# Kernel tuning notes

Measured on AMD Instinct MI355X. Metric: run time of the kernel, lower is better.

## Reference

```python
import jax, jax.numpy as jnp
import numpy as np

N = 50000      # nodes
E = 800000     # edges (avg degree 16)
F_IN = 128
H = 4          # heads
F_OUT = 64


def setup_inputs() -> dict:
    key = jax.random.key(0)
    ks = jax.random.split(key, 10)
    feat = jax.random.normal(ks[0], (N, F_IN), jnp.float32)
    src = jax.random.randint(ks[1], (E,), 0, N, dtype=jnp.int32)
    dst = jax.random.randint(ks[2], (E,), 0, N, dtype=jnp.int32)
    # fc: Linear(F_IN -> H*F_OUT, bias=False); torch weight layout [H*F_OUT, F_IN]
    fc_w = jax.random.normal(ks[3], (H * F_OUT, F_IN), jnp.float32) * (1.0 / np.sqrt(F_IN))
    # attention vectors live in input-feature space: (1, H, F_IN) -> store as (H, F_IN)
    attn_l = jax.random.normal(ks[4], (H, F_IN), jnp.float32) * 0.1
    attn_r = jax.random.normal(ks[5], (H, F_IN), jnp.float32) * 0.1
    attn_l1 = jax.random.normal(ks[6], (H, F_IN), jnp.float32) * 0.1
    attn_r1 = jax.random.normal(ks[7], (H, F_IN), jnp.float32) * 0.1
    bias = jax.random.normal(ks[8], (H * F_OUT,), jnp.float32) * 0.01
    return {"feat": feat, "src": src, "dst": dst, "fc_w": fc_w,
            "attn_l": attn_l, "attn_r": attn_r,
            "attn_l1": attn_l1, "attn_r1": attn_r1, "bias": bias}


def reference(feat, src, dst, fc_w, attn_l, attn_r, attn_l1, attn_r1, bias):
    n = feat.shape[0]
    h, f_out = attn_l.shape[0], fc_w.shape[0] // attn_l.shape[0]

    fs = feat[src]  # [E, F_in] gather
    fd = feat[dst]  # [E, F_in] gather

    # e1[e,h] = sum_f (feat[src]*attn_l)[h,f] * (feat[dst]*attn_r)[h,f]
    e1 = jnp.einsum('ef,ef,hf->eh', fs, fd, attn_l * attn_r)
    # e2 same with attn_l1/attn_r1
    e2 = jnp.einsum('ef,ef,hf->eh', fs, fd, attn_l1 * attn_r1)
    # e3 = ||feat[src]*attn_l1||^2 + ||feat[dst]*attn_r1||^2 (per node, then gathered)
    el2 = jnp.einsum('nf,hf->nh', feat * feat, attn_l1 * attn_l1)  # [N, H]
    er2 = jnp.einsum('nf,hf->nh', feat * feat, attn_r1 * attn_r1)  # [N, H]

    e = e1 - 2.0 * e2 + el2[src] + er2[dst]  # [E, H] squared-distance score

    # edge_softmax: softmax over incoming edges of each destination node
    m = jax.ops.segment_max(e, dst, num_segments=n)          # [N, H]
    ex = jnp.exp(e - m[dst])                                  # [E, H]
    denom = jax.ops.segment_sum(ex, dst, num_segments=n)     # [N, H]
    a = ex / denom[dst]                                       # [E, H]

    # feature projection then u_mul_e + sum aggregation
    ft = (feat @ fc_w.T).reshape(n, h, f_out)                 # [N, H, F_out]
    rst = jax.ops.segment_sum(ft[src] * a[:, :, None], dst, num_segments=n)

    return rst + bias.reshape(1, h, f_out)
```

## Files before the change

kernel.cpp:

```cpp
#include <hip/hip_runtime.h>

#define N_NODES 50000
#define F_IN    128
#define CAP     64
#define C_OUT   256
#define EDGE_BLOCKS 3125
#define W_BLOCKS    32
#define NODE_BLOCKS 12500

typedef short bf16x8 __attribute__((ext_vector_type(8)));
typedef float f32x4  __attribute__((ext_vector_type(4)));

__device__ __forceinline__ unsigned short f2bf(float f) {
    union { float f; unsigned u; } v; v.f = f;
    return (unsigned short)((v.u + 0x7FFFu + ((v.u >> 16) & 1u)) >> 16);
}
__device__ __forceinline__ float asf(unsigned u) { union { unsigned u; float f; } v; v.u = u; return v.f; }
__device__ __forceinline__ void unp8(uint4 u, float* f) {
    f[0] = asf(u.x << 16); f[1] = asf(u.x & 0xffff0000u);
    f[2] = asf(u.y << 16); f[3] = asf(u.y & 0xffff0000u);
    f[4] = asf(u.z << 16); f[5] = asf(u.z & 0xffff0000u);
    f[6] = asf(u.w << 16); f[7] = asf(u.w & 0xffff0000u);
}

__global__ __launch_bounds__(256) void k_prep(const float* __restrict__ feat,
                                              const float* __restrict__ fcw,
                                              const float* __restrict__ al1,
                                              const int* __restrict__ src,
                                              const int* __restrict__ dst,
                                              int* __restrict__ deg,
                                              int* __restrict__ esrc,
                                              unsigned short* __restrict__ fb16,
                                              unsigned short* __restrict__ wb16,
                                              float* __restrict__ el2) {
    int bid = blockIdx.x, t = threadIdx.x;
    if (bid < EDGE_BLOCKS) {
        int e = bid * 256 + t;
        int d = dst[e];
        int pos = atomicAdd(&deg[d], 1);
        if (pos < CAP) esrc[(size_t)d * CAP + pos] = src[e];
    } else if (bid < EDGE_BLOCKS + W_BLOCKS) {
        int j = (bid - EDGE_BLOCKS) * 256 + t;
        float4 v = ((const float4*)fcw)[j];
        ushort4 o = { f2bf(v.x), f2bf(v.y), f2bf(v.z), f2bf(v.w) };
        ((ushort4*)wb16)[j] = o;
    } else {
        int r = (bid - EDGE_BLOCKS - W_BLOCKS) * 4 + (t >> 6);
        int l = t & 63, h = l & 3, cb = l >> 2;
        const float4* fr = (const float4*)(feat + (size_t)r * F_IN + cb * 8);
        float4 f0 = fr[0], f1 = fr[1];
        const float4* ap = (const float4*)(al1 + h * F_IN + cb * 8);
        float4 a0 = ap[0], a1 = ap[1];
        float p = 0.f;
        p = fmaf(f0.x * f0.x, a0.x * a0.x, p);
        p = fmaf(f0.y * f0.y, a0.y * a0.y, p);
        p = fmaf(f0.z * f0.z, a0.z * a0.z, p);
        p = fmaf(f0.w * f0.w, a0.w * a0.w, p);
        p = fmaf(f1.x * f1.x, a1.x * a1.x, p);
        p = fmaf(f1.y * f1.y, a1.y * a1.y, p);
        p = fmaf(f1.z * f1.z, a1.z * a1.z, p);
        p = fmaf(f1.w * f1.w, a1.w * a1.w, p);
#pragma unroll
        for (int o = 4; o < 64; o <<= 1) p += __shfl_xor(p, o, 64);
        if (cb == 0) el2[r * 4 + h] = p;
        if (h == 0) {
            uint4 o4;
            o4.x = (unsigned)f2bf(f0.x) | ((unsigned)f2bf(f0.y) << 16);
            o4.y = (unsigned)f2bf(f0.z) | ((unsigned)f2bf(f0.w) << 16);
            o4.z = (unsigned)f2bf(f1.x) | ((unsigned)f2bf(f1.y) << 16);
            o4.w = (unsigned)f2bf(f1.z) | ((unsigned)f2bf(f1.w) << 16);
            ((uint4*)fb16)[(size_t)r * 16 + cb] = o4;
        }
    }
}

__global__ __launch_bounds__(256) void k_fused(const unsigned short* __restrict__ fb16,
                                               const unsigned short* __restrict__ wb16,
                                               const float* __restrict__ al, const float* __restrict__ ar,
                                               const float* __restrict__ al1, const float* __restrict__ ar1,
                                               const int* __restrict__ esrc,
                                               const int* __restrict__ degv,
                                               const float* __restrict__ el2,
                                               const float* __restrict__ bias,
                                               float* __restrict__ out) {
    __shared__ float s_w2[512];
    __shared__ float s_bias[256];
    __shared__ unsigned short s_af[16 * 136];
    __shared__ unsigned short s_fs[4][16 * 136];

    int t = threadIdx.x;
    for (int i = t; i < 512; i += 256)
        s_w2[i] = al[i] * ar[i] - 2.0f * al1[i] * ar1[i];
    s_bias[t] = bias[t];
    __syncthreads();

    int w = t >> 6, l = t & 63, g = l >> 4, ecol = l & 15;
    int d = __builtin_amdgcn_readfirstlane(blockIdx.x * 4 + w);
    int deg = degv[d]; if (deg > CAP) deg = CAP;
    const int* ep = esrc + d * CAP;

    uint4 wfr[4];
    {
        int hc = ecol & 3;
        bool hv = ecol < 4;
#pragma unroll
        for (int s = 0; s < 4; ++s) {
            uint4 u = ((const uint4*)fb16)[d * 16 + s * 4 + g];
            float fd[8]; unp8(u, fd);
            int k0 = s * 32 + g * 8;
            float wv[8];
#pragma unroll
            for (int j = 0; j < 8; ++j)
                wv[j] = hv ? fd[j] * s_w2[hc * 128 + k0 + j] : 0.f;
            uint4 o;
            o.x = (unsigned)f2bf(wv[0]) | ((unsigned)f2bf(wv[1]) << 16);
            o.y = (unsigned)f2bf(wv[2]) | ((unsigned)f2bf(wv[3]) << 16);
            o.z = (unsigned)f2bf(wv[4]) | ((unsigned)f2bf(wv[5]) << 16);
            o.w = (unsigned)f2bf(wv[6]) | ((unsigned)f2bf(wv[7]) << 16);
            wfr[s] = o;
        }
    }

    float m = -3.4e38f, den = 0.f;
    f32x4 acc[8];
#pragma unroll
    for (int b = 0; b < 8; ++b) acc[b] = (f32x4){0.f, 0.f, 0.f, 0.f};

    for (int c0 = 0; c0 < deg; c0 += 16) {
        int4 i4 = *(const int4*)(ep + c0 + g * 4);
        unsigned er = (unsigned)ep[c0 + ecol];
        if (er >= N_NODES) er = 0;
        unsigned ce[4] = { (unsigned)i4.x, (unsigned)i4.y, (unsigned)i4.z, (unsigned)i4.w };
#pragma unroll
        for (int r = 0; r < 4; ++r) if (ce[r] >= N_NODES) ce[r] = 0;

        f32x4 sc;
#pragma unroll
        for (int r = 0; r < 4; ++r) sc[r] = el2[ce[r] * 4 + (ecol & 3)];

        uint4 fsr[4];
#pragma unroll
        for (int s = 0; s < 4; ++s)
            fsr[s] = ((const uint4*)fb16)[er * 16u + s * 4 + g];

#pragma unroll
        for (int s = 0; s < 4; ++s) {
            union { uint4 u; bf16x8 v; } a, b;
            a.u = fsr[s]; b.u = wfr[s];
            sc = __builtin_amdgcn_mfma_f32_16x16x32_bf16(a.v, b.v, sc, 0, 0, 0);
        }

#pragma unroll
        for (int s = 0; s < 4; ++s)
            *(uint4*)&s_fs[w][ecol * 136 + s * 32 + g * 8] = fsr[s];

        float s4[4];
#pragma unroll
        for (int r = 0; r < 4; ++r)
            s4[r] = (c0 + g * 4 + r < deg) ? sc[r] : -3.4e38f;
        float mx = fmaxf(fmaxf(s4[0], s4[1]), fmaxf(s4[2], s4[3]));
        mx = fmaxf(mx, __shfl_xor(mx, 16, 64));
        mx = fmaxf(mx, __shfl_xor(mx, 32, 64));
        float mn = fmaxf(m, mx);
        float rs = __expf(m - mn);
        den *= rs;
#pragma unroll
        for (int b = 0; b < 8; ++b) {
            acc[b][0] *= rs; acc[b][1] *= rs; acc[b][2] *= rs; acc[b][3] *= rs;
        }
        float p4[4], ps = 0.f;
#pragma unroll
        for (int r = 0; r < 4; ++r) { p4[r] = __expf(s4[r] - mn); ps += p4[r]; }
        ps += __shfl_xor(ps, 16, 64);
        ps += __shfl_xor(ps, 32, 64);
        den += ps;
        m = mn;

        union { uint4 u; bf16x8 v; } pf;
        pf.u.x = f2bf(p4[0]); pf.u.y = f2bf(p4[1]);
        pf.u.z = f2bf(p4[2]); pf.u.w = f2bf(p4[3]);

        __builtin_amdgcn_wave_barrier();
#pragma unroll
        for (int b = 0; b < 8; ++b) {
            union { uint4 u; bf16x8 v; } af;
            af.u.x = s_fs[w][(g * 4 + 0) * 136 + b * 16 + ecol];
            af.u.y = s_fs[w][(g * 4 + 1) * 136 + b * 16 + ecol];
            af.u.z = s_fs[w][(g * 4 + 2) * 136 + b * 16 + ecol];
            af.u.w = s_fs[w][(g * 4 + 3) * 136 + b * 16 + ecol];
            acc[b] = __builtin_amdgcn_mfma_f32_16x16x32_bf16(af.v, pf.v, acc[b], 0, 0, 0);
        }
        __builtin_amdgcn_wave_barrier();
    }

    float inv = (den > 0.f) ? 1.0f / den : 0.f;
    if (ecol < 4) {
        int row = w * 4 + ecol;
#pragma unroll
        for (int b = 0; b < 8; ++b) {
            unsigned lo = (unsigned)f2bf(acc[b][0] * inv) | ((unsigned)f2bf(acc[b][1] * inv) << 16);
            unsigned hi = (unsigned)f2bf(acc[b][2] * inv) | ((unsigned)f2bf(acc[b][3] * inv) << 16);
            uint2 o; o.x = lo; o.y = hi;
            *(uint2*)&s_af[row * 136 + b * 16 + g * 4] = o;
        }
    }
    __syncthreads();

    bf16x8 afr[4];
#pragma unroll
    for (int step = 0; step < 4; ++step)
        afr[step] = *(const bf16x8*)&s_af[ecol * 136 + step * 32 + g * 8];
    f32x4 c[4] = {};
#pragma unroll
    for (int h4 = 0; h4 < 4; ++h4) {
#pragma unroll
        for (int step = 0; step < 4; ++step) {
            union { uint4 u; bf16x8 v; } b;
            b.u = *(const uint4*)(wb16 + (size_t)(h4 * 64 + w * 16 + ecol) * 128 + step * 32 + g * 8);
            c[h4] = __builtin_amdgcn_mfma_f32_16x16x32_bf16(afr[step], b.v, c[h4], 0, 0, 0);
        }
    }
    int node = blockIdx.x * 4 + g;
#pragma unroll
    for (int h4 = 0; h4 < 4; ++h4)
        out[(size_t)node * 256 + h4 * 64 + w * 16 + ecol] = c[h4][h4] + s_bias[h4 * 64 + w * 16 + ecol];
}

extern "C" void kernel_launch(void* const* d_in, const int* in_sizes, int n_in,
                              void* d_out, int out_size, void* d_ws, size_t ws_size,
                              hipStream_t stream) {
    const float* feat = (const float*)d_in[0];
    const int*   src  = (const int*)d_in[1];
    const int*   dst  = (const int*)d_in[2];
    const float* fcw  = (const float*)d_in[3];
    const float* al   = (const float*)d_in[4];
    const float* ar   = (const float*)d_in[5];
    const float* al1  = (const float*)d_in[6];
    const float* ar1  = (const float*)d_in[7];
    const float* bias = (const float*)d_in[8];
    float* out = (float*)d_out;

    char* ws = (char*)d_ws;
    size_t o = 0;
    auto take = [&](size_t b) -> void* {
        void* p = ws + o;
        o = (o + b + 255) & ~(size_t)255;
        return p;
    };
    unsigned short* wb16 = (unsigned short*)take((size_t)C_OUT * F_IN * 2);
    unsigned short* fb16 = (unsigned short*)take((size_t)N_NODES * F_IN * 2);
    int*   esrc = (int*)take((size_t)N_NODES * CAP * 4);
    int*   deg  = (int*)take((size_t)N_NODES * 4);
    float* el2  = (float*)take((size_t)N_NODES * 4 * 4);

    hipMemsetAsync(deg, 0, (size_t)N_NODES * 4, stream);
    k_prep<<<EDGE_BLOCKS + W_BLOCKS + NODE_BLOCKS, 256, 0, stream>>>(
        feat, fcw, al1, src, dst, deg, esrc, fb16, wb16, el2);
    k_fused<<<N_NODES / 4, 256, 0, stream>>>(
        fb16, wb16, al, ar, al1, ar1, esrc, deg, el2, bias, out);
}
```

Measured before the change: 318.9 us.

## Prefetch next neighbor chunk, swizzle LDS, per-wave output projection, vectorize edge scatter

The edge-binning pass now handles four edges per thread using int4 loads. The fused kernel software-pipelines neighbor gathers by loading the next 16-edge chunk's feature rows and el2 scores during the current chunk's compute. The s_fs shared-memory layout is XOR-style swizzled to reduce bank conflicts on the transposed reads. The final projection runs per wave on its own node, replacing the block-level __syncthreads with a wave barrier, at the cost of four times more MFMAs and weight loads per wave. A dead dummy weight-load loop is also left in.

```diff
diff --git a/kernel.cpp b/kernel.cpp
--- a/kernel.cpp
+++ b/kernel.cpp
@@ -1,11 +1,12 @@
 #include <hip/hip_runtime.h>
 
 #define N_NODES 50000
+#define N_EDGES 800000
 #define F_IN    128
 #define CAP     64
 #define C_OUT   256
-#define EDGE_BLOCKS 3125
-#define W_BLOCKS    32
+#define EB4     782
+#define W_BLOCKS 32
 #define NODE_BLOCKS 12500
 
 typedef short bf16x8 __attribute__((ext_vector_type(8)));
@@ -34,18 +35,27 @@
                                               unsigned short* __restrict__ wb16,
                                               float* __restrict__ el2) {
     int bid = blockIdx.x, t = threadIdx.x;
-    if (bid < EDGE_BLOCKS) {
-        int e = bid * 256 + t;
-        int d = dst[e];
-        int pos = atomicAdd(&deg[d], 1);
-        if (pos < CAP) esrc[(size_t)d * CAP + pos] = src[e];
-    } else if (bid < EDGE_BLOCKS + W_BLOCKS) {
-        int j = (bid - EDGE_BLOCKS) * 256 + t;
+    if (bid < EB4) {
+        int e0 = (bid * 256 + t) * 4;
+        if (e0 < N_EDGES) {
+            int4 d4 = *(const int4*)(dst + e0);
+            int4 s4 = *(const int4*)(src + e0);
+            int p0 = atomicAdd(&deg[d4.x], 1);
+            int p1 = atomicAdd(&deg[d4.y], 1);
+            int p2 = atomicAdd(&deg[d4.z], 1);
+            int p3 = atomicAdd(&deg[d4.w], 1);
+            if (p0 < CAP) esrc[d4.x * CAP + p0] = s4.x;
+            if (p1 < CAP) esrc[d4.y * CAP + p1] = s4.y;
+            if (p2 < CAP) esrc[d4.z * CAP + p2] = s4.z;
+            if (p3 < CAP) esrc[d4.w * CAP + p3] = s4.w;
+        }
+    } else if (bid < EB4 + W_BLOCKS) {
+        int j = (bid - EB4) * 256 + t;
         float4 v = ((const float4*)fcw)[j];
         ushort4 o = { f2bf(v.x), f2bf(v.y), f2bf(v.z), f2bf(v.w) };
         ((ushort4*)wb16)[j] = o;
     } else {
-        int r = (bid - EDGE_BLOCKS - W_BLOCKS) * 4 + (t >> 6);
+        int r = (bid - EB4 - W_BLOCKS) * 4 + (t >> 6);
         int l = t & 63, h = l & 3, cb = l >> 2;
         const float4* fr = (const float4*)(feat + (size_t)r * F_IN + cb * 8);
         float4 f0 = fr[0], f1 = fr[1];
@@ -85,7 +95,7 @@
                                                float* __restrict__ out) {
     __shared__ float s_w2[512];
     __shared__ float s_bias[256];
-    __shared__ unsigned short s_af[16 * 136];
+    __shared__ unsigned short s_af[4][4 * 136];
     __shared__ unsigned short s_fs[4][16 * 136];
 
     int t = threadIdx.x;
@@ -98,6 +108,25 @@
     int d = __builtin_amdgcn_readfirstlane(blockIdx.x * 4 + w);
     int deg = degv[d]; if (deg > CAP) deg = CAP;
     const int* ep = esrc + d * CAP;
+    int nch = (deg + 15) >> 4;
+
+    int4 i4 = *(const int4*)(ep + g * 4);
+    unsigned er = (unsigned)ep[ecol];
+    uint4 ud[4];
+#pragma unroll
+    for (int s = 0; s < 4; ++s) ud[s] = ((const uint4*)fb16)[d * 16 + s * 4 + g];
+
+    if (er >= N_NODES) er = 0;
+    unsigned ce[4] = { (unsigned)i4.x, (unsigned)i4.y, (unsigned)i4.z, (unsigned)i4.w };
+#pragma unroll
+    for (int r = 0; r < 4; ++r) if (ce[r] >= N_NODES) ce[r] = 0;
+
+    uint4 fsr[4];
+#pragma unroll
+    for (int s = 0; s < 4; ++s) fsr[s] = ((const uint4*)fb16)[er * 16u + s * 4 + g];
+    float e2g[4];
+#pragma unroll
+    for (int r = 0; r < 4; ++r) e2g[r] = el2[ce[r] * 4 + (ecol & 3)];
 
     uint4 wfr[4];
     {
@@ -105,8 +134,7 @@
         bool hv = ecol < 4;
 #pragma unroll
         for (int s = 0; s < 4; ++s) {
-            uint4 u = ((const uint4*)fb16)[d * 16 + s * 4 + g];
-            float fd[8]; unp8(u, fd);
+            float fd[8]; unp8(ud[s], fd);
             int k0 = s * 32 + g * 8;
             float wv[8];
 #pragma unroll
@@ -126,23 +154,17 @@
 #pragma unroll
     for (int b = 0; b < 8; ++b) acc[b] = (f32x4){0.f, 0.f, 0.f, 0.f};
 
-    for (int c0 = 0; c0 < deg; c0 += 16) {
-        int4 i4 = *(const int4*)(ep + c0 + g * 4);
-        unsigned er = (unsigned)ep[c0 + ecol];
-        if (er >= N_NODES) er = 0;
-        unsigned ce[4] = { (unsigned)i4.x, (unsigned)i4.y, (unsigned)i4.z, (unsigned)i4.w };
-#pragma unroll
-        for (int r = 0; r < 4; ++r) if (ce[r] >= N_NODES) ce[r] = 0;
+    for (int c = 0; c < nch; ++c) {
+        bool more = (c + 1 < nch);
+        int4 i4n = i4; unsigned ern = 0;
+        if (more) {
+            i4n = *(const int4*)(ep + (c + 1) * 16 + g * 4);
+            ern = (unsigned)ep[(c + 1) * 16 + ecol];
+        }
 
         f32x4 sc;
 #pragma unroll
-        for (int r = 0; r < 4; ++r) sc[r] = el2[ce[r] * 4 + (ecol & 3)];
-
-        uint4 fsr[4];
-#pragma unroll
-        for (int s = 0; s < 4; ++s)
-            fsr[s] = ((const uint4*)fb16)[er * 16u + s * 4 + g];
-
+        for (int r = 0; r < 4; ++r) sc[r] = e2g[r];
 #pragma unroll
         for (int s = 0; s < 4; ++s) {
             union { uint4 u; bf16x8 v; } a, b;
@@ -151,13 +173,27 @@
         }
 
 #pragma unroll
-        for (int s = 0; s < 4; ++s)
-            *(uint4*)&s_fs[w][ecol * 136 + s * 32 + g * 8] = fsr[s];
+        for (int s = 0; s < 4; ++s) {
+            int cs = ((s * 4 + g) + 2 * (ecol >> 2)) & 15;
+            *(uint4*)&s_fs[w][ecol * 136 + cs * 8] = fsr[s];
+        }
+
+        uint4 fsrn[4]; float e2gn[4];
+        if (more) {
+            if (ern >= N_NODES) ern = 0;
+            unsigned cen[4] = { (unsigned)i4n.x, (unsigned)i4n.y, (unsigned)i4n.z, (unsigned)i4n.w };
+#pragma unroll
+            for (int r = 0; r < 4; ++r) if (cen[r] >= N_NODES) cen[r] = 0;
+#pragma unroll
+            for (int s = 0; s < 4; ++s) fsrn[s] = ((const uint4*)fb16)[ern * 16u + s * 4 + g];
+#pragma unroll
+            for (int r = 0; r < 4; ++r) e2gn[r] = el2[cen[r] * 4 + (ecol & 3)];
+        }
 
         float s4[4];
 #pragma unroll
         for (int r = 0; r < 4; ++r)
-            s4[r] = (c0 + g * 4 + r < deg) ? sc[r] : -3.4e38f;
+            s4[r] = (c * 16 + g * 4 + r < deg) ? sc[r] : -3.4e38f;
         float mx = fmaxf(fmaxf(s4[0], s4[1]), fmaxf(s4[2], s4[3]));
         mx = fmaxf(mx, __shfl_xor(mx, 16, 64));
         mx = fmaxf(mx, __shfl_xor(mx, 32, 64));
@@ -183,47 +219,77 @@
         __builtin_amdgcn_wave_barrier();
 #pragma unroll
         for (int b = 0; b < 8; ++b) {
+            int cs = ((2 * b + (ecol >> 3)) + 2 * g) & 15;
+            int off = cs * 8 + (ecol & 7);
             union { uint4 u; bf16x8 v; } af;
-            af.u.x = s_fs[w][(g * 4 + 0) * 136 + b * 16 + ecol];
-            af.u.y = s_fs[w][(g * 4 + 1) * 136 + b * 16 + ecol];
-            af.u.z = s_fs[w][(g * 4 + 2) * 136 + b * 16 + ecol];
-            af.u.w = s_fs[w][(g * 4 + 3) * 136 + b * 16 + ecol];
+            af.u.x = s_fs[w][(g * 4 + 0) * 136 + off];
+            af.u.y = s_fs[w][(g * 4 + 1) * 136 + off];
+            af.u.z = s_fs[w][(g * 4 + 2) * 136 + off];
+            af.u.w = s_fs[w][(g * 4 + 3) * 136 + off];
             acc[b] = __builtin_amdgcn_mfma_f32_16x16x32_bf16(af.v, pf.v, acc[b], 0, 0, 0);
         }
         __builtin_amdgcn_wave_barrier();
+
+        if (more) {
+#pragma unroll
+            for (int s = 0; s < 4; ++s) fsr[s] = fsrn[s];
+#pragma unroll
+            for (int r = 0; r < 4; ++r) e2g[r] = e2gn[r];
+        }
     }
 
     float inv = (den > 0.f) ? 1.0f / den : 0.f;
     if (ecol < 4) {
-        int row = w * 4 + ecol;
 #pragma unroll
         for (int b = 0; b < 8; ++b) {
             unsigned lo = (unsigned)f2bf(acc[b][0] * inv) | ((unsigned)f2bf(acc[b][1] * inv) << 16);
             unsigned hi = (unsigned)f2bf(acc[b][2] * inv) | ((unsigned)f2bf(acc[b][3] * inv) << 16);
             uint2 o; o.x = lo; o.y = hi;
-            *(uint2*)&s_af[row * 136 + b * 16 + g * 4] = o;
-        }
-    }
-    __syncthreads();
+            *(uint2*)&s_af[w][ecol * 136 + b * 16 + g * 4] = o;
+        }
+    }
+    __builtin_amdgcn_wave_barrier();
 
     bf16x8 afr[4];
 #pragma unroll
     for (int step = 0; step < 4; ++step)
-        afr[step] = *(const bf16x8*)&s_af[ecol * 136 + step * 32 + g * 8];
-    f32x4 c[4] = {};
-#pragma unroll
-    for (int h4 = 0; h4 < 4; ++h4) {
+        afr[step] = *(const bf16x8*)&s_af[w][(ecol & 3) * 136 + step * 32 + g * 8];
+    f32x4 c4[4] = {};
+#pragma unroll
+    for (int ct = 0; ct < 4; ++ct) {
 #pragma unroll
         for (int step = 0; step < 4; ++step) {
             union { uint4 u; bf16x8 v; } b;
-            b.u = *(const uint4*)(wb16 + (size_t)(h4 * 64 + w * 16 + ecol) * 128 + step * 32 + g * 8);
-            c[h4] = __builtin_amdgcn_mfma_f32_16x16x32_bf16(afr[step], b.v, c[h4], 0, 0, 0);
-        }
-    }
-    int node = blockIdx.x * 4 + g;
-#pragma unroll
-    for (int h4 = 0; h4 < 4; ++h4)
-        out[(size_t)node * 256 + h4 * 64 + w * 16 + ecol] = c[h4][h4] + s_bias[h4 * 64 + w * 16 + ecol];
+            b.u = *(const uint4*)(wb16 + (size_t)(ct * 64 + 0) * 128);
+            (void)b;
+        }
+    }
+#pragma unroll
+    for (int h4 = 0; h4 < 4; ++h4) {
+        f32x4 cc = {};
+#pragma unroll
+        for (int step = 0; step < 4; ++step) {
+            union { uint4 u; bf16x8 v; } b;
+            b.u = *(const uint4*)(wb16 + (size_t)(h4 * 64 + 0 * 16 + ecol) * 128 + step * 32 + g * 8);
+            cc = __builtin_amdgcn_mfma_f32_16x16x32_bf16(afr[step], b.v, cc, 0, 0, 0);
+        }
+        f32x4 cc1 = {}, cc2 = {}, cc3 = {};
+#pragma unroll
+        for (int step = 0; step < 4; ++step) {
+            union { uint4 u; bf16x8 v; } b1, b2, b3;
+            b1.u = *(const uint4*)(wb16 + (size_t)(h4 * 64 + 1 * 16 + ecol) * 128 + step * 32 + g * 8);
+            cc1 = __builtin_amdgcn_mfma_f32_16x16x32_bf16(afr[step], b1.v, cc1, 0, 0, 0);
+            b2.u = *(const uint4*)(wb16 + (size_t)(h4 * 64 + 2 * 16 + ecol) * 128 + step * 32 + g * 8);
+            cc2 = __builtin_amdgcn_mfma_f32_16x16x32_bf16(afr[step], b2.v, cc2, 0, 0, 0);
+            b3.u = *(const uint4*)(wb16 + (size_t)(h4 * 64 + 3 * 16 + ecol) * 128 + step * 32 + g * 8);
+            cc3 = __builtin_amdgcn_mfma_f32_16x16x32_bf16(afr[step], b3.v, cc3, 0, 0, 0);
+        }
+        f32x4 mine = cc;
+        if (g == 1) mine = cc1;
+        if (g == 2) mine = cc2;
+        if (g == 3) mine = cc3;
+        out[(size_t)d * 256 + h4 * 64 + g * 16 + ecol] = mine[h4] + s_bias[h4 * 64 + g * 16 + ecol];
+    }
 }
 
 extern "C" void kernel_launch(void* const* d_in, const int* in_sizes, int n_in,
@@ -254,7 +320,7 @@
     float* el2  = (float*)take((size_t)N_NODES * 4 * 4);
 
     hipMemsetAsync(deg, 0, (size_t)N_NODES * 4, stream);
-    k_prep<<<EDGE_BLOCKS + W_BLOCKS + NODE_BLOCKS, 256, 0, stream>>>(
+    k_prep<<<EB4 + W_BLOCKS + NODE_BLOCKS, 256, 0, stream>>>(
         feat, fcw, al1, src, dst, deg, esrc, fb16, wb16, el2);
     k_fused<<<N_NODES / 4, 256, 0, stream>>>(
         fb16, wb16, al, ar, al1, ar1, esrc, deg, el2, bias, out);
```

Measured after the change: 603.1 us. +89.1%, slower.

## Fold el2 into MFMA score, prefetch next neighbor chunk, vectorize edge bucketing

Applied to the files above, without the earlier changes.

Removes the per-node el2 precomputation and its gather. The squared-norm term is now computed inside the score MFMA by squaring the gathered source features and multiplying them against al1^2 fragments. Gathers of the next chunk of neighbor features are software-prefetched so they overlap the softmax and aggregation MFMAs. The prep kernel now buckets four edges per thread with int4 loads and becomes a plain bf16 conversion. This costs extra registers, four more MFMAs per chunk, and bf16 precision on the squared term.

```diff
diff --git a/kernel.cpp b/kernel.cpp
--- a/kernel.cpp
+++ b/kernel.cpp
@@ -1,12 +1,13 @@
 #include <hip/hip_runtime.h>
 
 #define N_NODES 50000
+#define N_EDGES 800000
 #define F_IN    128
 #define CAP     64
 #define C_OUT   256
-#define EDGE_BLOCKS 3125
-#define W_BLOCKS    32
-#define NODE_BLOCKS 12500
+#define EB4     782
+#define W_BLOCKS 32
+#define CVT_BLOCKS 6250
 
 typedef short bf16x8 __attribute__((ext_vector_type(8)));
 typedef float f32x4  __attribute__((ext_vector_type(4)));
@@ -25,52 +26,37 @@
 
 __global__ __launch_bounds__(256) void k_prep(const float* __restrict__ feat,
                                               const float* __restrict__ fcw,
-                                              const float* __restrict__ al1,
                                               const int* __restrict__ src,
                                               const int* __restrict__ dst,
                                               int* __restrict__ deg,
                                               int* __restrict__ esrc,
                                               unsigned short* __restrict__ fb16,
-                                              unsigned short* __restrict__ wb16,
-                                              float* __restrict__ el2) {
+                                              unsigned short* __restrict__ wb16) {
     int bid = blockIdx.x, t = threadIdx.x;
-    if (bid < EDGE_BLOCKS) {
-        int e = bid * 256 + t;
-        int d = dst[e];
-        int pos = atomicAdd(&deg[d], 1);
-        if (pos < CAP) esrc[(size_t)d * CAP + pos] = src[e];
-    } else if (bid < EDGE_BLOCKS + W_BLOCKS) {
-        int j = (bid - EDGE_BLOCKS) * 256 + t;
+    if (bid < EB4) {
+        int e0 = (bid * 256 + t) * 4;
+        if (e0 < N_EDGES) {
+            int4 d4 = *(const int4*)(dst + e0);
+            int4 s4 = *(const int4*)(src + e0);
+            int p0 = atomicAdd(&deg[d4.x], 1);
+            int p1 = atomicAdd(&deg[d4.y], 1);
+            int p2 = atomicAdd(&deg[d4.z], 1);
+            int p3 = atomicAdd(&deg[d4.w], 1);
+            if (p0 < CAP) esrc[d4.x * CAP + p0] = s4.x;
+            if (p1 < CAP) esrc[d4.y * CAP + p1] = s4.y;
+            if (p2 < CAP) esrc[d4.z * CAP + p2] = s4.z;
+            if (p3 < CAP) esrc[d4.w * CAP + p3] = s4.w;
+        }
+    } else if (bid < EB4 + W_BLOCKS) {
+        int j = (bid - EB4) * 256 + t;
         float4 v = ((const float4*)fcw)[j];
         ushort4 o = { f2bf(v.x), f2bf(v.y), f2bf(v.z), f2bf(v.w) };
         ((ushort4*)wb16)[j] = o;
     } else {
-        int r = (bid - EDGE_BLOCKS - W_BLOCKS) * 4 + (t >> 6);
-        int l = t & 63, h = l & 3, cb = l >> 2;
-        const float4* fr = (const float4*)(feat + (size_t)r * F_IN + cb * 8);
-        float4 f0 = fr[0], f1 = fr[1];
-        const float4* ap = (const float4*)(al1 + h * F_IN + cb * 8);
-        float4 a0 = ap[0], a1 = ap[1];
-        float p = 0.f;
-        p = fmaf(f0.x * f0.x, a0.x * a0.x, p);
-        p = fmaf(f0.y * f0.y, a0.y * a0.y, p);
-        p = fmaf(f0.z * f0.z, a0.z * a0.z, p);
-        p = fmaf(f0.w * f0.w, a0.w * a0.w, p);
-        p = fmaf(f1.x * f1.x, a1.x * a1.x, p);
-        p = fmaf(f1.y * f1.y, a1.y * a1.y, p);
-        p = fmaf(f1.z * f1.z, a1.z * a1.z, p);
-        p = fmaf(f1.w * f1.w, a1.w * a1.w, p);
-#pragma unroll
-        for (int o = 4; o < 64; o <<= 1) p += __shfl_xor(p, o, 64);
-        if (cb == 0) el2[r * 4 + h] = p;
-        if (h == 0) {
-            uint4 o4;
-            o4.x = (unsigned)f2bf(f0.x) | ((unsigned)f2bf(f0.y) << 16);
-            o4.y = (unsigned)f2bf(f0.z) | ((unsigned)f2bf(f0.w) << 16);
-            o4.z = (unsigned)f2bf(f1.x) | ((unsigned)f2bf(f1.y) << 16);
-            o4.w = (unsigned)f2bf(f1.z) | ((unsigned)f2bf(f1.w) << 16);
-            ((uint4*)fb16)[(size_t)r * 16 + cb] = o4;
-        }
+        int i = (bid - EB4 - W_BLOCKS) * 256 + t;
+        float4 v = ((const float4*)feat)[i];
+        ushort4 o = { f2bf(v.x), f2bf(v.y), f2bf(v.z), f2bf(v.w) };
+        ((ushort4*)fb16)[i] = o;
     }
 }
 
@@ -80,17 +66,19 @@
                                                const float* __restrict__ al1, const float* __restrict__ ar1,
                                                const int* __restrict__ esrc,
                                                const int* __restrict__ degv,
-                                               const float* __restrict__ el2,
                                                const float* __restrict__ bias,
                                                float* __restrict__ out) {
     __shared__ float s_w2[512];
+    __shared__ float s_wl2[512];
     __shared__ float s_bias[256];
     __shared__ unsigned short s_af[16 * 136];
     __shared__ unsigned short s_fs[4][16 * 136];
 
     int t = threadIdx.x;
-    for (int i = t; i < 512; i += 256)
-        s_w2[i] = al[i] * ar[i] - 2.0f * al1[i] * ar1[i];
+    for (int i = t; i < 512; i += 256) {
+        s_w2[i]  = al[i] * ar[i] - 2.0f * al1[i] * ar1[i];
+        s_wl2[i] = al1[i] * al1[i];
+    }
     s_bias[t] = bias[t];
     __syncthreads();
 
@@ -98,26 +86,42 @@
     int d = __builtin_amdgcn_readfirstlane(blockIdx.x * 4 + w);
     int deg = degv[d]; if (deg > CAP) deg = CAP;
     const int* ep = esrc + d * CAP;
-
-    uint4 wfr[4];
+    int nch = (deg + 15) >> 4;
+
+    unsigned er = (unsigned)ep[ecol];
+    uint4 ud[4];
+#pragma unroll
+    for (int s = 0; s < 4; ++s) ud[s] = ((const uint4*)fb16)[d * 16 + s * 4 + g];
+    if (er >= N_NODES) er = 0;
+
+    uint4 fsr[4];
+#pragma unroll
+    for (int s = 0; s < 4; ++s) fsr[s] = ((const uint4*)fb16)[er * 16u + s * 4 + g];
+
+    uint4 wfr[4], b2fr[4];
     {
         int hc = ecol & 3;
         bool hv = ecol < 4;
 #pragma unroll
         for (int s = 0; s < 4; ++s) {
-            uint4 u = ((const uint4*)fb16)[d * 16 + s * 4 + g];
-            float fd[8]; unp8(u, fd);
+            float fd[8]; unp8(ud[s], fd);
             int k0 = s * 32 + g * 8;
-            float wv[8];
-#pragma unroll
-            for (int j = 0; j < 8; ++j)
+            float wv[8], bv[8];
+#pragma unroll
+            for (int j = 0; j < 8; ++j) {
                 wv[j] = hv ? fd[j] * s_w2[hc * 128 + k0 + j] : 0.f;
-            uint4 o;
-            o.x = (unsigned)f2bf(wv[0]) | ((unsigned)f2bf(wv[1]) << 16);
-            o.y = (unsigned)f2bf(wv[2]) | ((unsigned)f2bf(wv[3]) << 16);
-            o.z = (unsigned)f2bf(wv[4]) | ((unsigned)f2bf(wv[5]) << 16);
-            o.w = (unsigned)f2bf(wv[6]) | ((unsigned)f2bf(wv[7]) << 16);
-            wfr[s] = o;
+                bv[j] = hv ? s_wl2[hc * 128 + k0 + j] : 0.f;
+            }
+            uint4 o, o2;
+            o.x  = (unsigned)f2bf(wv[0]) | ((unsigned)f2bf(wv[1]) << 16);
+            o.y  = (unsigned)f2bf(wv[2]) | ((unsigned)f2bf(wv[3]) << 16);
+            o.z  = (unsigned)f2bf(wv[4]) | ((unsigned)f2bf(wv[5]) << 16);
+            o.w  = (unsigned)f2bf(wv[6]) | ((unsigned)f2bf(wv[7]) << 16);
+            o2.x = (unsigned)f2bf(bv[0]) | ((unsigned)f2bf(bv[1]) << 16);
+            o2.y = (unsigned)f2bf(bv[2]) | ((unsigned)f2bf(bv[3]) << 16);
+            o2.z = (unsigned)f2bf(bv[4]) | ((unsigned)f2bf(bv[5]) << 16);
+            o2.w = (unsigned)f2bf(bv[6]) | ((unsigned)f2bf(bv[7]) << 16);
+            wfr[s] = o; b2fr[s] = o2;
         }
     }
 
@@ -126,38 +130,51 @@
 #pragma unroll
     for (int b = 0; b < 8; ++b) acc[b] = (f32x4){0.f, 0.f, 0.f, 0.f};
 
-    for (int c0 = 0; c0 < deg; c0 += 16) {
-        int4 i4 = *(const int4*)(ep + c0 + g * 4);
-        unsigned er = (unsigned)ep[c0 + ecol];
-        if (er >= N_NODES) er = 0;
-        unsigned ce[4] = { (unsigned)i4.x, (unsigned)i4.y, (unsigned)i4.z, (unsigned)i4.w };
-#pragma unroll
-        for (int r = 0; r < 4; ++r) if (ce[r] >= N_NODES) ce[r] = 0;
-
-        f32x4 sc;
-#pragma unroll
-        for (int r = 0; r < 4; ++r) sc[r] = el2[ce[r] * 4 + (ecol & 3)];
-
-        uint4 fsr[4];
-#pragma unroll
-        for (int s = 0; s < 4; ++s)
-            fsr[s] = ((const uint4*)fb16)[er * 16u + s * 4 + g];
-
+    for (int c = 0; c < nch; ++c) {
+        bool more = (c + 1 < nch);
+        unsigned ern = more ? (unsigned)ep[(c + 1) * 16 + ecol] : 0u;
+
+        uint4 fsq[4];
+#pragma unroll
+        for (int s = 0; s < 4; ++s) {
+            float f[8]; unp8(fsr[s], f);
+            uint4 o;
+            o.x = (unsigned)f2bf(f[0] * f[0]) | ((unsigned)f2bf(f[1] * f[1]) << 16);
+            o.y = (unsigned)f2bf(f[2] * f[2]) | ((unsigned)f2bf(f[3] * f[3]) << 16);
+            o.z = (unsigned)f2bf(f[4] * f[4]) | ((unsigned)f2bf(f[5] * f[5]) << 16);
+            o.w = (unsigned)f2bf(f[6] * f[6]) | ((unsigned)f2bf(f[7] * f[7]) << 16);
+            fsq[s] = o;
+        }
+
+        f32x4 sc = (f32x4){0.f, 0.f, 0.f, 0.f};
 #pragma unroll
         for (int s = 0; s < 4; ++s) {
             union { uint4 u; bf16x8 v; } a, b;
             a.u = fsr[s]; b.u = wfr[s];
             sc = __builtin_amdgcn_mfma_f32_16x16x32_bf16(a.v, b.v, sc, 0, 0, 0);
         }
+#pragma unroll
+        for (int s = 0; s < 4; ++s) {
+            union { uint4 u; bf16x8 v; } a, b;
+            a.u = fsq[s]; b.u = b2fr[s];
+            sc = __builtin_amdgcn_mfma_f32_16x16x32_bf16(a.v, b.v, sc, 0, 0, 0);
+        }
 
 #pragma unroll
         for (int s = 0; s < 4; ++s)
             *(uint4*)&s_fs[w][ecol * 136 + s * 32 + g * 8] = fsr[s];
 
+        uint4 fsrn[4];
+        if (more) {
+            if (ern >= N_NODES) ern = 0;
+#pragma unroll
+            for (int s = 0; s < 4; ++s) fsrn[s] = ((const uint4*)fb16)[ern * 16u + s * 4 + g];
+        }
+
         float s4[4];
 #pragma unroll
         for (int r = 0; r < 4; ++r)
-            s4[r] = (c0 + g * 4 + r < deg) ? sc[r] : -3.4e38f;
+            s4[r] = (c * 16 + g * 4 + r < deg) ? sc[r] : -3.4e38f;
         float mx = fmaxf(fmaxf(s4[0], s4[1]), fmaxf(s4[2], s4[3]));
         mx = fmaxf(mx, __shfl_xor(mx, 16, 64));
         mx = fmaxf(mx, __shfl_xor(mx, 32, 64));
@@ -191,6 +208,11 @@
             acc[b] = __builtin_amdgcn_mfma_f32_16x16x32_bf16(af.v, pf.v, acc[b], 0, 0, 0);
         }
         __builtin_amdgcn_wave_barrier();
+
+        if (more) {
+#pragma unroll
+            for (int s = 0; s < 4; ++s) fsr[s] = fsrn[s];
+        }
     }
 
     float inv = (den > 0.f) ? 1.0f / den : 0.f;
@@ -251,11 +273,10 @@
     unsigned short* fb16 = (unsigned short*)take((size_t)N_NODES * F_IN * 2);
     int*   esrc = (int*)take((size_t)N_NODES * CAP * 4);
     int*   deg  = (int*)take((size_t)N_NODES * 4);
-    float* el2  = (float*)take((size_t)N_NODES * 4 * 4);
 
     hipMemsetAsync(deg, 0, (size_t)N_NODES * 4, stream);
-    k_prep<<<EDGE_BLOCKS + W_BLOCKS + NODE_BLOCKS, 256, 0, stream>>>(
-        feat, fcw, al1, src, dst, deg, esrc, fb16, wb16, el2);
+    k_prep<<<EB4 + W_BLOCKS + CVT_BLOCKS, 256, 0, stream>>>(
+        feat, fcw, src, dst, deg, esrc, fb16, wb16);
     k_fused<<<N_NODES / 4, 256, 0, stream>>>(
-        fb16, wb16, al, ar, al1, ar1, esrc, deg, el2, bias, out);
-}
+        fb16, wb16, al, ar, al1, ar1, esrc, deg, bias, out);
+}
```

After: 369.2 us. +15.8%, slower.

## Split each node's edge loop across two waves and vectorize edge bucketing

Applied to the files above, without the earlier changes.

The fused kernel now runs 512 threads per block. Each destination node gets two waves that handle alternating 16-edge chunks, and their online-softmax partial states (max, denominator, accumulators) are merged through shared memory before the projection MFMA. This shortens the serial per-node edge loop and adds latency hiding, at the cost of an extra merge step, more shared memory, and half the waves sitting idle during projection. The prep kernel also processes four edges per thread with int4 loads, reducing the number of blocks and load instructions used for bucketing.

```diff
diff --git a/kernel.cpp b/kernel.cpp
--- a/kernel.cpp
+++ b/kernel.cpp
@@ -1,11 +1,12 @@
 #include <hip/hip_runtime.h>
 
 #define N_NODES 50000
+#define N_EDGES 800000
 #define F_IN    128
 #define CAP     64
 #define C_OUT   256
-#define EDGE_BLOCKS 3125
-#define W_BLOCKS    32
+#define EB4     782
+#define W_BLOCKS 32
 #define NODE_BLOCKS 12500
 
 typedef short bf16x8 __attribute__((ext_vector_type(8)));
@@ -34,18 +35,27 @@
                                               unsigned short* __restrict__ wb16,
                                               float* __restrict__ el2) {
     int bid = blockIdx.x, t = threadIdx.x;
-    if (bid < EDGE_BLOCKS) {
-        int e = bid * 256 + t;
-        int d = dst[e];
-        int pos = atomicAdd(&deg[d], 1);
-        if (pos < CAP) esrc[(size_t)d * CAP + pos] = src[e];
-    } else if (bid < EDGE_BLOCKS + W_BLOCKS) {
-        int j = (bid - EDGE_BLOCKS) * 256 + t;
+    if (bid < EB4) {
+        int e0 = (bid * 256 + t) * 4;
+        if (e0 < N_EDGES) {
+            int4 d4 = *(const int4*)(dst + e0);
+            int4 s4 = *(const int4*)(src + e0);
+            int p0 = atomicAdd(&deg[d4.x], 1);
+            int p1 = atomicAdd(&deg[d4.y], 1);
+            int p2 = atomicAdd(&deg[d4.z], 1);
+            int p3 = atomicAdd(&deg[d4.w], 1);
+            if (p0 < CAP) esrc[d4.x * CAP + p0] = s4.x;
+            if (p1 < CAP) esrc[d4.y * CAP + p1] = s4.y;
+            if (p2 < CAP) esrc[d4.z * CAP + p2] = s4.z;
+            if (p3 < CAP) esrc[d4.w * CAP + p3] = s4.w;
+        }
+    } else if (bid < EB4 + W_BLOCKS) {
+        int j = (bid - EB4) * 256 + t;
         float4 v = ((const float4*)fcw)[j];
         ushort4 o = { f2bf(v.x), f2bf(v.y), f2bf(v.z), f2bf(v.w) };
         ((ushort4*)wb16)[j] = o;
     } else {
-        int r = (bid - EDGE_BLOCKS - W_BLOCKS) * 4 + (t >> 6);
+        int r = (bid - EB4 - W_BLOCKS) * 4 + (t >> 6);
         int l = t & 63, h = l & 3, cb = l >> 2;
         const float4* fr = (const float4*)(feat + (size_t)r * F_IN + cb * 8);
         float4 f0 = fr[0], f1 = fr[1];
@@ -74,7 +84,7 @@
     }
 }
 
-__global__ __launch_bounds__(256) void k_fused(const unsigned short* __restrict__ fb16,
+__global__ __launch_bounds__(512, 6) void k_fused(const unsigned short* __restrict__ fb16,
                                                const unsigned short* __restrict__ wb16,
                                                const float* __restrict__ al, const float* __restrict__ ar,
                                                const float* __restrict__ al1, const float* __restrict__ ar1,
@@ -86,16 +96,16 @@
     __shared__ float s_w2[512];
     __shared__ float s_bias[256];
     __shared__ unsigned short s_af[16 * 136];
-    __shared__ unsigned short s_fs[4][16 * 136];
+    __shared__ unsigned short s_fs[8][16 * 136];
 
     int t = threadIdx.x;
-    for (int i = t; i < 512; i += 256)
-        s_w2[i] = al[i] * ar[i] - 2.0f * al1[i] * ar1[i];
-    s_bias[t] = bias[t];
+    s_w2[t] = al[t] * ar[t] - 2.0f * al1[t] * ar1[t];
+    if (t < 256) s_bias[t] = bias[t];
     __syncthreads();
 
     int w = t >> 6, l = t & 63, g = l >> 4, ecol = l & 15;
-    int d = __builtin_amdgcn_readfirstlane(blockIdx.x * 4 + w);
+    int nb = w >> 1, half = w & 1;
+    int d = __builtin_amdgcn_readfirstlane(blockIdx.x * 4 + nb);
     int deg = degv[d]; if (deg > CAP) deg = CAP;
     const int* ep = esrc + d * CAP;
 
@@ -126,7 +136,7 @@
 #pragma unroll
     for (int b = 0; b < 8; ++b) acc[b] = (f32x4){0.f, 0.f, 0.f, 0.f};
 
-    for (int c0 = 0; c0 < deg; c0 += 16) {
+    for (int c0 = half * 16; c0 < deg; c0 += 32) {
         int4 i4 = *(const int4*)(ep + c0 + g * 4);
         unsigned er = (unsigned)ep[c0 + ecol];
         if (er >= N_NODES) er = 0;
@@ -193,37 +203,60 @@
         __builtin_amdgcn_wave_barrier();
     }
 
-    float inv = (den > 0.f) ? 1.0f / den : 0.f;
-    if (ecol < 4) {
-        int row = w * 4 + ecol;
-#pragma unroll
-        for (int b = 0; b < 8; ++b) {
-            unsigned lo = (unsigned)f2bf(acc[b][0] * inv) | ((unsigned)f2bf(acc[b][1] * inv) << 16);
-            unsigned hi = (unsigned)f2bf(acc[b][2] * inv) | ((unsigned)f2bf(acc[b][3] * inv) << 16);
-            uint2 o; o.x = lo; o.y = hi;
+    if (half == 1 && ecol < 4) {
+        float* cmb = (float*)&s_fs[w][0];
+#pragma unroll
+        for (int b = 0; b < 8; ++b) {
+            cmb[ecol * 128 + b * 16 + g * 4 + 0] = acc[b][0];
+            cmb[ecol * 128 + b * 16 + g * 4 + 1] = acc[b][1];
+            cmb[ecol * 128 + b * 16 + g * 4 + 2] = acc[b][2];
+            cmb[ecol * 128 + b * 16 + g * 4 + 3] = acc[b][3];
+        }
+        if (g == 0) { cmb[512 + ecol] = m; cmb[516 + ecol] = den; }
+    }
+    __syncthreads();
+    if (half == 0 && ecol < 4) {
+        const float* pc = (const float*)&s_fs[w + 1][0];
+        float m1 = pc[512 + ecol], den1 = pc[516 + ecol];
+        float M = fmaxf(m, m1);
+        float r0 = __expf(m - M), r1 = __expf(m1 - M);
+        float dn = den * r0 + den1 * r1;
+        float iv = (dn > 0.f) ? 1.0f / dn : 0.f;
+        int row = nb * 4 + ecol;
+#pragma unroll
+        for (int b = 0; b < 8; ++b) {
+            float a0 = (acc[b][0] * r0 + pc[ecol * 128 + b * 16 + g * 4 + 0] * r1) * iv;
+            float a1 = (acc[b][1] * r0 + pc[ecol * 128 + b * 16 + g * 4 + 1] * r1) * iv;
+            float a2 = (acc[b][2] * r0 + pc[ecol * 128 + b * 16 + g * 4 + 2] * r1) * iv;
+            float a3 = (acc[b][3] * r0 + pc[ecol * 128 + b * 16 + g * 4 + 3] * r1) * iv;
+            uint2 o;
+            o.x = (unsigned)f2bf(a0) | ((unsigned)f2bf(a1) << 16);
+            o.y = (unsigned)f2bf(a2) | ((unsigned)f2bf(a3) << 16);
             *(uint2*)&s_af[row * 136 + b * 16 + g * 4] = o;
         }
     }
     __syncthreads();
 
-    bf16x8 afr[4];
-#pragma unroll
-    for (int step = 0; step < 4; ++step)
-        afr[step] = *(const bf16x8*)&s_af[ecol * 136 + step * 32 + g * 8];
-    f32x4 c[4] = {};
-#pragma unroll
-    for (int h4 = 0; h4 < 4; ++h4) {
-#pragma unroll
-        for (int step = 0; step < 4; ++step) {
-            union { uint4 u; bf16x8 v; } b;
-            b.u = *(const uint4*)(wb16 + (size_t)(h4 * 64 + w * 16 + ecol) * 128 + step * 32 + g * 8);
-            c[h4] = __builtin_amdgcn_mfma_f32_16x16x32_bf16(afr[step], b.v, c[h4], 0, 0, 0);
-        }
-    }
-    int node = blockIdx.x * 4 + g;
-#pragma unroll
-    for (int h4 = 0; h4 < 4; ++h4)
-        out[(size_t)node * 256 + h4 * 64 + w * 16 + ecol] = c[h4][h4] + s_bias[h4 * 64 + w * 16 + ecol];
+    if (w < 4) {
+        bf16x8 afr[4];
+#pragma unroll
+        for (int step = 0; step < 4; ++step)
+            afr[step] = *(const bf16x8*)&s_af[ecol * 136 + step * 32 + g * 8];
+        f32x4 c[4] = {};
+#pragma unroll
+        for (int h4 = 0; h4 < 4; ++h4) {
+#pragma unroll
+            for (int step = 0; step < 4; ++step) {
+                union { uint4 u; bf16x8 v; } b;
+                b.u = *(const uint4*)(wb16 + (size_t)(h4 * 64 + w * 16 + ecol) * 128 + step * 32 + g * 8);
+                c[h4] = __builtin_amdgcn_mfma_f32_16x16x32_bf16(afr[step], b.v, c[h4], 0, 0, 0);
+            }
+        }
+        int node = blockIdx.x * 4 + g;
+#pragma unroll
+        for (int h4 = 0; h4 < 4; ++h4)
+            out[(size_t)node * 256 + h4 * 64 + w * 16 + ecol] = c[h4][h4] + s_bias[h4 * 64 + w * 16 + ecol];
+    }
 }
 
 extern "C" void kernel_launch(void* const* d_in, const int* in_sizes, int n_in,
@@ -254,8 +287,8 @@
     float* el2  = (float*)take((size_t)N_NODES * 4 * 4);
 
     hipMemsetAsync(deg, 0, (size_t)N_NODES * 4, stream);
-    k_prep<<<EDGE_BLOCKS + W_BLOCKS + NODE_BLOCKS, 256, 0, stream>>>(
+    k_prep<<<EB4 + W_BLOCKS + NODE_BLOCKS, 256, 0, stream>>>(
         feat, fcw, al1, src, dst, deg, esrc, fb16, wb16, el2);
-    k_fused<<<N_NODES / 4, 256, 0, stream>>>(
+    k_fused<<<N_NODES / 4, 512, 0, stream>>>(
         fb16, wb16, al, ar, al1, ar1, esrc, deg, el2, bias, out);
 }
```

Result: slower. 381.3 us (+19.5%).
